# Optimization experiments

Measured on AMD Instinct MI355X. Metric: run time of the kernel, lower is better.

The kernel has to match this reference:

```python
import jax, jax.numpy as jnp
import numpy as np

NUM_HEADS = 4
HIDDEN = 384

def _l2norm(t, eps=1e-12):
    # torch.nn.functional.normalize(dim=-1): x / max(||x||_2, eps)
    n = jnp.sqrt(jnp.sum(t * t, axis=-1, keepdims=True))
    return t / jnp.maximum(n, eps)

def setup_inputs() -> dict:
    key = jax.random.key(0)
    k1, k2, k3, k4 = jax.random.split(key, 4)
    B, N, C = 4, 16384, HIDDEN
    x = jax.random.normal(k1, (B, N, C), dtype=jnp.float32)
    W_qkv = jax.random.normal(k2, (3 * C, C), dtype=jnp.float32) * 0.02  # torch Linear weight [out,in], no bias
    temperature_ch = jnp.ones((NUM_HEADS, 1, 1), dtype=jnp.float32)
    W_out = jax.random.normal(k3, (C, C), dtype=jnp.float32) * 0.02
    b_out = jax.random.normal(k4, (C,), dtype=jnp.float32) * 0.02
    return {"x": x, "W_qkv": W_qkv, "temperature_ch": temperature_ch,
            "W_out": W_out, "b_out": b_out,
            "B_in": 4, "C_in": C, "H": 32, "W": 32, "D": 16}

def reference(x, W_qkv, temperature_ch, W_out, b_out, B_in, C_in, H, W, D):
    B, N, C = x.shape
    h = NUM_HEADS
    d = C // h
    # qkv projection: (B,N,3C) -> (3,B,h,N,d)
    qkv = (x @ W_qkv.T).reshape(B, N, 3, h, d).transpose(2, 0, 3, 1, 4)
    q, k, v = qkv[0], qkv[1], qkv[2]
    # transpose token/channel axes: (B,h,d,N)
    q = jnp.swapaxes(q, -2, -1)
    k = jnp.swapaxes(k, -2, -1)
    v = jnp.swapaxes(v, -2, -1)
    # L2-normalize over tokens (last axis)
    q = _l2norm(q)
    k = _l2norm(k)
    # channel attention: (B,h,d,d)
    attn = jnp.einsum('bhcn,bhdn->bhcd', q, k)
    attn = attn * temperature_ch  # (h,1,1) broadcasts over (B,h,d,d)
    attn = jax.nn.softmax(attn, axis=-1)
    # (B,h,d,N) -> (B,N,h,d) -> (B,N,C)
    x_CA = jnp.einsum('bhcd,bhdn->bhcn', attn, v)
    x_CA = x_CA.transpose(0, 3, 1, 2).reshape(B, N, C)
    return x_CA @ W_out.T + b_out
```

## Files before the change

### kernel.cpp

```cpp
#include <hip/hip_runtime.h>
#include <math.h>


#define B_    4
#define NTOK  16384
#define C_    384
#define NH    4
#define DH    96

typedef __attribute__((ext_vector_type(8))) short short8;
typedef __attribute__((ext_vector_type(4))) float f32x4;
typedef __attribute__((ext_vector_type(4))) unsigned short ushort4v;
typedef __attribute__((ext_vector_type(8))) unsigned short ushort8v;
typedef __attribute__((ext_vector_type(4))) unsigned int uint4v;

#define XH_B   0ull
#define XHT_B  50331648ull
#define GP_B   100663296ull
#define G_B    138412032ull
#define P_B    140771328ull
#define SSQ_B  145489920ull
#define ATT_B  145502208ull
#define T_B    146092032ull
#define MPH_B  150810624ull

__device__ inline unsigned short f2bf(float f) {
    unsigned u = __float_as_uint(f);
    u += 0x7FFFu + ((u >> 16) & 1u);
    return (unsigned short)(u >> 16);
}

__device__ inline void load16(const void* g, void* l) {
    __builtin_amdgcn_global_load_lds(
        (const __attribute__((address_space(1))) unsigned int*)g,
        (__attribute__((address_space(3))) unsigned int*)l, 16, 0, 0);
}

__global__ __launch_bounds__(256) void k_conv(const float* __restrict__ X,
                                              unsigned short* __restrict__ Xh,
                                              unsigned short* __restrict__ XhT) {
    __shared__ __align__(16) unsigned int Tp[64 * 33];
    const int tid = threadIdx.x;
    const int t0 = blockIdx.x * 64, c0 = blockIdx.y * 64, b = blockIdx.z;
    const int tp = tid >> 4, cg = tid & 15;
#pragma unroll
    for (int i = 0; i < 2; ++i) {
        const int tpair = tp + 16 * i;
        const int t = t0 + tpair * 2;
        const float4 v0 = *(const float4*)(X + ((size_t)(b * NTOK + t))     * C_ + c0 + cg * 4);
        const float4 v1 = *(const float4*)(X + ((size_t)(b * NTOK + t + 1)) * C_ + c0 + cg * 4);
        const unsigned short h00 = f2bf(v0.x), h01 = f2bf(v0.y), h02 = f2bf(v0.z), h03 = f2bf(v0.w);
        const unsigned short h10 = f2bf(v1.x), h11 = f2bf(v1.y), h12 = f2bf(v1.z), h13 = f2bf(v1.w);
        ushort4v a; a.x = h00; a.y = h01; a.z = h02; a.w = h03;
        ushort4v c; c.x = h10; c.y = h11; c.z = h12; c.w = h13;
        *(ushort4v*)(Xh + ((size_t)(b * NTOK + t))     * C_ + c0 + cg * 4) = a;
        *(ushort4v*)(Xh + ((size_t)(b * NTOK + t + 1)) * C_ + c0 + cg * 4) = c;
        Tp[(cg * 4 + 0) * 33 + tpair] = (unsigned)h00 | ((unsigned)h10 << 16);
        Tp[(cg * 4 + 1) * 33 + tpair] = (unsigned)h01 | ((unsigned)h11 << 16);
        Tp[(cg * 4 + 2) * 33 + tpair] = (unsigned)h02 | ((unsigned)h12 << 16);
        Tp[(cg * 4 + 3) * 33 + tpair] = (unsigned)h03 | ((unsigned)h13 << 16);
    }
    __syncthreads();
    const int c = tid >> 2, seg = tid & 3;
    unsigned int w[8];
#pragma unroll
    for (int k = 0; k < 8; ++k) w[k] = Tp[c * 33 + seg * 8 + k];
    unsigned int* dst = (unsigned int*)(XhT + ((size_t)(b * C_ + c0 + c)) * NTOK + t0 + seg * 16);
    uint4v s0; s0.x = w[0]; s0.y = w[1]; s0.z = w[2]; s0.w = w[3];
    uint4v s1; s1.x = w[4]; s1.y = w[5]; s1.z = w[6]; s1.w = w[7];
    *(uint4v*)dst       = s0;
    *((uint4v*)dst + 1) = s1;
}

__global__ __launch_bounds__(256, 2) void k_gram_mfma(const unsigned short* __restrict__ XhT,
                                                      float* __restrict__ Gpart) {
    __shared__ __align__(16) unsigned char sm[32768];
    const int l = blockIdx.x;
    const int xcd = l & 7, slot = l >> 3;
    const int grp = xcd * 8 + slot / 6, tile = slot % 6;
    const int chunk = grp >> 2, b = grp & 3;
    const int ti = (tile == 0) ? 0 : (tile < 3 ? 1 : 2);
    const int tj = tile - (ti * (ti + 1)) / 2;
    const int tid = threadIdx.x;
    const int lane = tid & 63, wid = tid >> 6;
    const int wr = wid >> 1, wc = wid & 1;

    const int e = (lane & 7) ^ (lane >> 3);
    const int rsub = lane >> 3;

    const size_t rowb = (size_t)NTOK * 2;
    const unsigned char* Abase = (const unsigned char*)XhT + (size_t)(b * C_ + ti * 128) * rowb;
    const unsigned char* Bbase = (const unsigned char*)XhT + (size_t)(b * C_ + tj * 128) * rowb;

    f32x4 acc[4][4];
#pragma unroll
    for (int i = 0; i < 4; i++)
#pragma unroll
        for (int j = 0; j < 4; j++) acc[i][j] = (f32x4)(0.f);

    for (int ks = 0; ks < 16; ++ks) {
        const size_t colb = (size_t)(chunk * 1024 + ks * 64) * 2 + (size_t)e * 16;
        __syncthreads();
#pragma unroll
        for (int call = 0; call < 4; ++call) {
            const int row = wid * 32 + call * 8 + rsub;
            load16(Abase + (size_t)row * rowb + colb, sm + (wid * 32 + call * 8) * 128);
            load16(Bbase + (size_t)row * rowb + colb, sm + 16384 + (wid * 32 + call * 8) * 128);
        }
        __syncthreads();
#pragma unroll
        for (int p = 0; p < 2; ++p) {
            const int s = p * 4 + (lane >> 4);
            short8 av[4], bv[4];
#pragma unroll
            for (int fi = 0; fi < 4; ++fi) {
                const int c = wr * 64 + fi * 16 + (lane & 15);
                av[fi] = *(const short8*)(sm + c * 128 + ((s ^ (c & 7)) << 4));
            }
#pragma unroll
            for (int fj = 0; fj < 4; ++fj) {
                const int c = wc * 64 + fj * 16 + (lane & 15);
                bv[fj] = *(const short8*)(sm + 16384 + c * 128 + ((s ^ (c & 7)) << 4));
            }
#pragma unroll
            for (int fi = 0; fi < 4; ++fi)
#pragma unroll
                for (int fj = 0; fj < 4; ++fj)
                    acc[fi][fj] = __builtin_amdgcn_mfma_f32_16x16x32_bf16(av[fi], bv[fj], acc[fi][fj], 0, 0, 0);
        }
    }
    float* gp = Gpart + (size_t)grp * (C_ * C_);
    const int r0 = (lane >> 4) * 4, cc = lane & 15;
#pragma unroll
    for (int fi = 0; fi < 4; ++fi) {
        const int ci = ti * 128 + wr * 64 + fi * 16 + r0;
#pragma unroll
        for (int fj = 0; fj < 4; ++fj) {
            const int cj = tj * 128 + wc * 64 + fj * 16 + cc;
#pragma unroll
            for (int r = 0; r < 4; ++r)
                gp[(size_t)(ci + r) * C_ + cj] = acc[fi][fj][r];
        }
    }
    if (ti != tj) {
#pragma unroll
        for (int fi = 0; fi < 4; ++fi) {
            const int cib = ti * 128 + wr * 64 + fi * 16 + r0;
#pragma unroll
            for (int fj = 0; fj < 4; ++fj) {
                const int cjb = tj * 128 + wc * 64 + fj * 16 + cc;
                *(f32x4*)(gp + (size_t)cjb * C_ + cib) = acc[fi][fj];
            }
        }
    }
}

__global__ __launch_bounds__(256) void k_reduceG(const float* __restrict__ Gpart,
                                                 float* __restrict__ G) {
    const size_t eo = ((size_t)blockIdx.x * 256 + threadIdx.x) * 4;
    float4 s = *(const float4*)(Gpart + eo);
#pragma unroll
    for (int c = 1; c < 16; ++c) {
        const float4 v = *(const float4*)(Gpart + (size_t)c * (B_ * C_ * C_) + eo);
        s.x += v.x; s.y += v.y; s.z += v.z; s.w += v.w;
    }
    *(float4*)(G + eo) = s;
}

__global__ __launch_bounds__(256) void k_P64(const float* __restrict__ Wqkv,
                                             const float* __restrict__ G,
                                             float* __restrict__ P) {
    __shared__ float As[32][65];
    __shared__ float Bs[32][65];
    const int tid = threadIdx.x;
    const int sel = blockIdx.z & 1, b = blockIdx.z >> 1;
    const int m0 = blockIdx.x * 64, n0 = blockIdx.y * 64;
    const float* A  = Wqkv + (size_t)sel * C_ * C_;
    const float* Bm = G + (size_t)b * C_ * C_;
    const int lr = tid >> 2, lk = (tid & 3) * 8;
    const int tm = (tid & 15) * 4, tn = (tid >> 4) * 4;
    float acc[4][4];
#pragma unroll
    for (int i = 0; i < 4; i++)
#pragma unroll
        for (int j = 0; j < 4; j++) acc[i][j] = 0.f;

    for (int k0 = 0; k0 < C_; k0 += 32) {
        float4 a0 = *(const float4*)(A  + (size_t)(m0 + lr) * C_ + k0 + lk);
        float4 a1 = *(const float4*)(A  + (size_t)(m0 + lr) * C_ + k0 + lk + 4);
        float4 b0 = *(const float4*)(Bm + (size_t)(n0 + lr) * C_ + k0 + lk);
        float4 b1 = *(const float4*)(Bm + (size_t)(n0 + lr) * C_ + k0 + lk + 4);
        __syncthreads();
        As[lk + 0][lr] = a0.x; As[lk + 1][lr] = a0.y; As[lk + 2][lr] = a0.z; As[lk + 3][lr] = a0.w;
        As[lk + 4][lr] = a1.x; As[lk + 5][lr] = a1.y; As[lk + 6][lr] = a1.z; As[lk + 7][lr] = a1.w;
        Bs[lk + 0][lr] = b0.x; Bs[lk + 1][lr] = b0.y; Bs[lk + 2][lr] = b0.z; Bs[lk + 3][lr] = b0.w;
        Bs[lk + 4][lr] = b1.x; Bs[lk + 5][lr] = b1.y; Bs[lk + 6][lr] = b1.z; Bs[lk + 7][lr] = b1.w;
        __syncthreads();
#pragma unroll
        for (int k = 0; k < 32; k++) {
            float a[4], bb[4];
            *(float4*)&a[0]  = *(const float4*)&As[k][tm];
            *(float4*)&bb[0] = *(const float4*)&Bs[k][tn];
#pragma unroll
            for (int i = 0; i < 4; i++)
#pragma unroll
                for (int j = 0; j < 4; j++)
                    acc[i][j] = fmaf(a[i], bb[j], acc[i][j]);
        }
    }
    float* outp = P + ((size_t)(sel * B_ + b) * C_ + m0 + tm) * C_ + n0 + tn;
#pragma unroll
    for (int i = 0; i < 4; i++) {
        float4 c0 = make_float4(acc[i][0], acc[i][1], acc[i][2], acc[i][3]);
        *(float4*)(outp + (size_t)i * C_) = c0;
    }
}

__global__ __launch_bounds__(256) void k_diag(const float* __restrict__ P,
                                              const float* __restrict__ Wqkv,
                                              float* __restrict__ ssq) {
    int g = blockIdx.x * 256 + threadIdx.x;
    int sel = g / (B_ * C_), rem = g % (B_ * C_), b = rem / C_, c = rem % C_;
    const float* pr = P + ((size_t)(sel * B_ + b) * C_ + c) * C_;
    const float* wr = Wqkv + ((size_t)sel * C_ + c) * C_;
    float s = 0.f;
#pragma unroll 4
    for (int k = 0; k < C_; k += 4) {
        float4 pv = *(const float4*)(pr + k);
        float4 wv = *(const float4*)(wr + k);
        s += pv.x * wv.x + pv.y * wv.y + pv.z * wv.z + pv.w * wv.w;
    }
    ssq[g] = s;
}

__global__ __launch_bounds__(256) void k_S(const float* __restrict__ P,
                                           const float* __restrict__ Wqkv,
                                           float* __restrict__ S) {
    __shared__ float Ps[32 * 97];
    __shared__ float Ks[32 * 17];
    const int cs = blockIdx.x, bh = blockIdx.y;
    const int b = bh >> 2, h = bh & 3;
    const int tid = threadIdx.x;
    const int ti = tid & 15, tj = tid >> 4;
    const float* P1 = P + ((size_t)b * C_ + h * DH) * C_;
    const float* Wk = Wqkv + ((size_t)(C_ + h * DH + cs * 16)) * C_;
    float acc[6];
#pragma unroll
    for (int i = 0; i < 6; i++) acc[i] = 0.f;

    for (int k0 = 0; k0 < C_; k0 += 32) {
        __syncthreads();
#pragma unroll
        for (int j = 0; j < 3; j++) {
            int f = tid + 256 * j;
            int row = f >> 3, q = f & 7;
            float4 v = *(const float4*)(P1 + (size_t)row * C_ + k0 + q * 4);
            Ps[(q * 4 + 0) * 97 + row] = v.x;
            Ps[(q * 4 + 1) * 97 + row] = v.y;
            Ps[(q * 4 + 2) * 97 + row] = v.z;
            Ps[(q * 4 + 3) * 97 + row] = v.w;
        }
        {
            int row = tid >> 4, kk = (tid & 15) * 2;
            float2 w = *(const float2*)(Wk + (size_t)row * C_ + k0 + kk);
            Ks[(kk + 0) * 17 + row] = w.x;
            Ks[(kk + 1) * 17 + row] = w.y;
        }
        __syncthreads();
#pragma unroll
        for (int k = 0; k < 32; k++) {
            const float bb = Ks[k * 17 + tj];
#pragma unroll
            for (int i = 0; i < 6; i++)
                acc[i] = fmaf(Ps[k * 97 + ti * 6 + i], bb, acc[i]);
        }
    }
    float* Sb = S + (size_t)bh * DH * DH;
#pragma unroll
    for (int i = 0; i < 6; i++)
        Sb[(size_t)(ti * 6 + i) * DH + cs * 16 + tj] = acc[i];
}

__global__ __launch_bounds__(128) void k_soft(float* __restrict__ S,
                                              const float* __restrict__ ssq,
                                              const float* __restrict__ temp) {
    __shared__ float rnk[DH];
    const int bh = blockIdx.x;
    const int b = bh >> 2, h = bh & 3;
    const int r = threadIdx.x;
    if (r < DH)
        rnk[r] = 1.f / fmaxf(sqrtf(ssq[B_ * C_ + b * C_ + h * DH + r]), 1e-12f);
    __syncthreads();
    if (r >= DH) return;
    const float rnq = temp[h] / fmaxf(sqrtf(ssq[b * C_ + h * DH + r]), 1e-12f);
    float* row = S + (size_t)bh * DH * DH + (size_t)r * DH;
    float rv[DH];
    float m = -1e30f;
#pragma unroll
    for (int d = 0; d < DH; d++) {
        rv[d] = row[d] * rnq * rnk[d];
        m = fmaxf(m, rv[d]);
    }
    float s = 0.f;
#pragma unroll
    for (int d = 0; d < DH; d++) { rv[d] = __expf(rv[d] - m); s += rv[d]; }
    const float inv = 1.f / s;
#pragma unroll
    for (int d = 0; d < DH; d++) row[d] = rv[d] * inv;
}

__global__ __launch_bounds__(128) void k_T(const float* __restrict__ attn,
                                           const float* __restrict__ Wqkv,
                                           float* __restrict__ T) {
    const int ck = blockIdx.x * 128 + threadIdx.x;
    const int y = blockIdx.y;
    const int b = y / C_, hc = y % C_, h = hc / DH, c = hc % DH;
    const float* ar = attn + ((size_t)(b * NH + h) * DH + c) * DH;
    const float* wv = Wqkv + ((size_t)(2 * C_ + h * DH)) * C_ + ck;
    float s = 0.f;
#pragma unroll 8
    for (int d = 0; d < DH; d++) s = fmaf(ar[d], wv[(size_t)d * C_], s);
    T[((size_t)b * C_ + hc) * C_ + ck] = s;
}

__global__ __launch_bounds__(256) void k_Mp64(const float* __restrict__ Wout,
                                              const float* __restrict__ T,
                                              unsigned short* __restrict__ Mph) {
    __shared__ float As[32][65];
    __shared__ float Bs[32][65];
    const int tid = threadIdx.x;
    const int b = blockIdx.z;
    const int m0 = blockIdx.x * 64, n0 = blockIdx.y * 64;
    const float* Tb = T + (size_t)b * C_ * C_;
    const int la_r = tid >> 2, la_k = (tid & 3) * 8;
    const int lb_k = tid >> 3, lb_c = (tid & 7) * 8;
    const int tm = (tid & 15) * 4, tn = (tid >> 4) * 4;
    float acc[4][4];
#pragma unroll
    for (int i = 0; i < 4; i++)
#pragma unroll
        for (int j = 0; j < 4; j++) acc[i][j] = 0.f;

    for (int k0 = 0; k0 < C_; k0 += 32) {
        float4 a0 = *(const float4*)(Wout + (size_t)(m0 + la_r) * C_ + k0 + la_k);
        float4 a1 = *(const float4*)(Wout + (size_t)(m0 + la_r) * C_ + k0 + la_k + 4);
        float4 b0 = *(const float4*)(Tb + (size_t)(k0 + lb_k) * C_ + n0 + lb_c);
        float4 b1 = *(const float4*)(Tb + (size_t)(k0 + lb_k) * C_ + n0 + lb_c + 4);
        __syncthreads();
        As[la_k + 0][la_r] = a0.x; As[la_k + 1][la_r] = a0.y; As[la_k + 2][la_r] = a0.z; As[la_k + 3][la_r] = a0.w;
        As[la_k + 4][la_r] = a1.x; As[la_k + 5][la_r] = a1.y; As[la_k + 6][la_r] = a1.z; As[la_k + 7][la_r] = a1.w;
        *(float4*)&Bs[lb_k][lb_c]     = b0;
        *(float4*)&Bs[lb_k][lb_c + 4] = b1;
        __syncthreads();
#pragma unroll
        for (int k = 0; k < 32; k++) {
            float a[4], bb[4];
            *(float4*)&a[0]  = *(const float4*)&As[k][tm];
            *(float4*)&bb[0] = *(const float4*)&Bs[k][tn];
#pragma unroll
            for (int i = 0; i < 4; i++)
#pragma unroll
                for (int j = 0; j < 4; j++)
                    acc[i][j] = fmaf(a[i], bb[j], acc[i][j]);
        }
    }
    unsigned short* outp = Mph + ((size_t)b * C_ + m0 + tm) * C_ + n0 + tn;
#pragma unroll
    for (int i = 0; i < 4; i++) {
        ushort4v h4;
        h4.x = f2bf(acc[i][0]); h4.y = f2bf(acc[i][1]);
        h4.z = f2bf(acc[i][2]); h4.w = f2bf(acc[i][3]);
        *(ushort4v*)(outp + (size_t)i * C_) = h4;
    }
}

__global__ __launch_bounds__(256, 2) void k_out_mfma(const unsigned short* __restrict__ Xh,
                                                     const unsigned short* __restrict__ Mph,
                                                     const float* __restrict__ bias,
                                                     float* __restrict__ out) {
    __shared__ __align__(16) unsigned char sm[32768];
    const int l = blockIdx.x;
    const int xcd = l & 7, k = l >> 3;
    const int mblk = xcd * 64 + k / 3, nblk = k % 3;
    const int m0 = mblk * 128, i0 = nblk * 128;
    const int b = mblk >> 7;
    const int tid = threadIdx.x;
    const int lane = tid & 63, wid = tid >> 6;
    const int wr = wid >> 1, wc = wid & 1;

    const int e = (lane & 7) ^ (lane >> 3);
    const int rsub = lane >> 3;

    const unsigned char* Abase = (const unsigned char*)Xh + (size_t)m0 * (C_ * 2);
    const unsigned char* Bbase = (const unsigned char*)Mph + (size_t)b * (C_ * C_ * 2) + (size_t)i0 * (C_ * 2);

    f32x4 acc[4][4];
#pragma unroll
    for (int i = 0; i < 4; i++)
#pragma unroll
        for (int j = 0; j < 4; j++) acc[i][j] = (f32x4)(0.f);

    for (int ks = 0; ks < 6; ++ks) {
        const size_t colb = (size_t)ks * 128 + (size_t)e * 16;
        __syncthreads();
#pragma unroll
        for (int call = 0; call < 4; ++call) {
            const int row = wid * 32 + call * 8 + rsub;
            load16(Abase + (size_t)row * (C_ * 2) + colb, sm + (wid * 32 + call * 8) * 128);
            load16(Bbase + (size_t)row * (C_ * 2) + colb, sm + 16384 + (wid * 32 + call * 8) * 128);
        }
        __syncthreads();
#pragma unroll
        for (int p = 0; p < 2; ++p) {
            const int s = p * 4 + (lane >> 4);
            short8 av[4], bv[4];
#pragma unroll
            for (int fi = 0; fi < 4; ++fi) {
                const int c = wr * 64 + fi * 16 + (lane & 15);
                av[fi] = *(const short8*)(sm + c * 128 + ((s ^ (c & 7)) << 4));
            }
#pragma unroll
            for (int fj = 0; fj < 4; ++fj) {
                const int c = wc * 64 + fj * 16 + (lane & 15);
                bv[fj] = *(const short8*)(sm + 16384 + c * 128 + ((s ^ (c & 7)) << 4));
            }
#pragma unroll
            for (int fi = 0; fi < 4; ++fi)
#pragma unroll
                for (int fj = 0; fj < 4; ++fj)
                    acc[fi][fj] = __builtin_amdgcn_mfma_f32_16x16x32_bf16(av[fi], bv[fj], acc[fi][fj], 0, 0, 0);
        }
    }
    const int r0 = (lane >> 4) * 4, cc = lane & 15;
#pragma unroll
    for (int fi = 0; fi < 4; ++fi) {
        const int m = m0 + wr * 64 + fi * 16 + r0;
#pragma unroll
        for (int fj = 0; fj < 4; ++fj) {
            const int ii = i0 + wc * 64 + fj * 16 + cc;
            const float bi = bias[ii];
#pragma unroll
            for (int r = 0; r < 4; ++r)
                out[(size_t)(m + r) * C_ + ii] = acc[fi][fj][r] + bi;
        }
    }
}

extern "C" void kernel_launch(void* const* d_in, const int* in_sizes, int n_in,
                              void* d_out, int out_size, void* d_ws, size_t ws_size,
                              hipStream_t stream) {
    const float* x    = (const float*)d_in[0];
    const float* Wqkv = (const float*)d_in[1];
    const float* temp = (const float*)d_in[2];
    const float* Wout = (const float*)d_in[3];
    const float* bout = (const float*)d_in[4];
    float* out = (float*)d_out;

    unsigned char* w8 = (unsigned char*)d_ws;
    unsigned short* Xh  = (unsigned short*)(w8 + XH_B);
    unsigned short* XhT = (unsigned short*)(w8 + XHT_B);
    float* Gpart = (float*)(w8 + GP_B);
    float* G     = (float*)(w8 + G_B);
    float* P     = (float*)(w8 + P_B);
    float* ssq   = (float*)(w8 + SSQ_B);
    float* Satt  = (float*)(w8 + ATT_B);
    float* T     = (float*)(w8 + T_B);
    unsigned short* Mph = (unsigned short*)(w8 + MPH_B);

    k_conv     <<<dim3(256, 6, B_), 256, 0, stream>>>(x, Xh, XhT);
    k_gram_mfma<<<dim3(384), 256, 0, stream>>>(XhT, Gpart);
    k_reduceG  <<<dim3(576), 256, 0, stream>>>(Gpart, G);
    k_P64      <<<dim3(6, 6, 2 * B_), 256, 0, stream>>>(Wqkv, G, P);
    k_diag     <<<dim3(12), 256, 0, stream>>>(P, Wqkv, ssq);
    k_S        <<<dim3(6, B_ * NH), 256, 0, stream>>>(P, Wqkv, Satt);
    k_soft     <<<dim3(B_ * NH), 128, 0, stream>>>(Satt, ssq, temp);
    k_T        <<<dim3(3, B_ * C_), 128, 0, stream>>>(Satt, Wqkv, T);
    k_Mp64     <<<dim3(6, 6, B_), 256, 0, stream>>>(Wout, T, Mph);
    k_out_mfma <<<dim3(1536), 256, 0, stream>>>(Xh, Mph, bout, out);
}
```

Measured before the change: 411.6 us.

## Split fp32-to-bf16 conversion from transpose and fold row-norm diag into softmax

Replaces the combined convert+transpose kernel with a flat grid-stride fp32-to-bf16 conversion kernel and a separate transpose kernel that reads the bf16 copy in 128x128 tiles. The aim is fully coalesced streaming of the fp32 input and wider transpose stores. It also removes the k_diag launch by computing the q/k squared norms inside k_soft, saving a launch but making 16 small blocks do the dot products serially. The extra pass re-reads the bf16 copy, which adds memory traffic.

```diff
diff --git a/kernel.cpp b/kernel.cpp
--- a/kernel.cpp
+++ b/kernel.cpp
@@ -19,7 +19,6 @@
 #define GP_B   100663296ull
 #define G_B    138412032ull
 #define P_B    140771328ull
-#define SSQ_B  145489920ull
 #define ATT_B  145502208ull
 #define T_B    146092032ull
 #define MPH_B  150810624ull
@@ -36,40 +35,50 @@
         (__attribute__((address_space(3))) unsigned int*)l, 16, 0, 0);
 }
 
-__global__ __launch_bounds__(256) void k_conv(const float* __restrict__ X,
-                                              unsigned short* __restrict__ Xh,
-                                              unsigned short* __restrict__ XhT) {
-    __shared__ __align__(16) unsigned int Tp[64 * 33];
-    const int tid = threadIdx.x;
-    const int t0 = blockIdx.x * 64, c0 = blockIdx.y * 64, b = blockIdx.z;
-    const int tp = tid >> 4, cg = tid & 15;
-#pragma unroll
-    for (int i = 0; i < 2; ++i) {
-        const int tpair = tp + 16 * i;
-        const int t = t0 + tpair * 2;
-        const float4 v0 = *(const float4*)(X + ((size_t)(b * NTOK + t))     * C_ + c0 + cg * 4);
-        const float4 v1 = *(const float4*)(X + ((size_t)(b * NTOK + t + 1)) * C_ + c0 + cg * 4);
-        const unsigned short h00 = f2bf(v0.x), h01 = f2bf(v0.y), h02 = f2bf(v0.z), h03 = f2bf(v0.w);
-        const unsigned short h10 = f2bf(v1.x), h11 = f2bf(v1.y), h12 = f2bf(v1.z), h13 = f2bf(v1.w);
-        ushort4v a; a.x = h00; a.y = h01; a.z = h02; a.w = h03;
-        ushort4v c; c.x = h10; c.y = h11; c.z = h12; c.w = h13;
-        *(ushort4v*)(Xh + ((size_t)(b * NTOK + t))     * C_ + c0 + cg * 4) = a;
-        *(ushort4v*)(Xh + ((size_t)(b * NTOK + t + 1)) * C_ + c0 + cg * 4) = c;
-        Tp[(cg * 4 + 0) * 33 + tpair] = (unsigned)h00 | ((unsigned)h10 << 16);
-        Tp[(cg * 4 + 1) * 33 + tpair] = (unsigned)h01 | ((unsigned)h11 << 16);
-        Tp[(cg * 4 + 2) * 33 + tpair] = (unsigned)h02 | ((unsigned)h12 << 16);
-        Tp[(cg * 4 + 3) * 33 + tpair] = (unsigned)h03 | ((unsigned)h13 << 16);
+__global__ __launch_bounds__(256) void k_convS(const float* __restrict__ X,
+                                               unsigned short* __restrict__ Xh) {
+    const size_t n4 = (size_t)B_ * NTOK * C_ / 4;
+    const size_t stride = (size_t)gridDim.x * 256;
+    for (size_t i = (size_t)blockIdx.x * 256 + threadIdx.x; i < n4; i += stride) {
+        const float4 v = *(const float4*)(X + i * 4);
+        ushort4v h;
+        h.x = f2bf(v.x); h.y = f2bf(v.y); h.z = f2bf(v.z); h.w = f2bf(v.w);
+        *(ushort4v*)(Xh + i * 4) = h;
+    }
+}
+
+__global__ __launch_bounds__(256) void k_trans(const unsigned short* __restrict__ Xh,
+                                               unsigned short* __restrict__ XhT) {
+    __shared__ unsigned int Tp[64 * 129];
+    const int tid = threadIdx.x;
+    const int t0 = blockIdx.x * 128, c0 = blockIdx.y * 128, b = blockIdx.z;
+    const int cg = tid & 15;
+#pragma unroll
+    for (int p = 0; p < 4; ++p) {
+        const int tp = (tid >> 4) + 16 * p;
+        const int t = t0 + tp * 2;
+        const ushort8v r0 = *(const ushort8v*)(Xh + ((size_t)(b * NTOK + t))     * C_ + c0 + cg * 8);
+        const ushort8v r1 = *(const ushort8v*)(Xh + ((size_t)(b * NTOK + t + 1)) * C_ + c0 + cg * 8);
+#pragma unroll
+        for (int j = 0; j < 8; ++j)
+            Tp[tp * 129 + cg * 8 + j] = (unsigned)r0[j] | ((unsigned)r1[j] << 16);
     }
     __syncthreads();
-    const int c = tid >> 2, seg = tid & 3;
-    unsigned int w[8];
-#pragma unroll
-    for (int k = 0; k < 8; ++k) w[k] = Tp[c * 33 + seg * 8 + k];
-    unsigned int* dst = (unsigned int*)(XhT + ((size_t)(b * C_ + c0 + c)) * NTOK + t0 + seg * 16);
-    uint4v s0; s0.x = w[0]; s0.y = w[1]; s0.z = w[2]; s0.w = w[3];
-    uint4v s1; s1.x = w[4]; s1.y = w[5]; s1.z = w[6]; s1.w = w[7];
-    *(uint4v*)dst       = s0;
-    *((uint4v*)dst + 1) = s1;
+    const int qtr = tid & 3;
+#pragma unroll
+    for (int p = 0; p < 2; ++p) {
+        const int c = (tid >> 2) + 64 * p;
+        unsigned int w[16];
+#pragma unroll
+        for (int m = 0; m < 16; ++m)
+            w[m] = Tp[(qtr * 16 + m) * 129 + c];
+        unsigned int* dst = (unsigned int*)(XhT + ((size_t)(b * C_ + c0 + c)) * NTOK + t0 + qtr * 32);
+#pragma unroll
+        for (int i = 0; i < 4; ++i) {
+            uint4v s4; s4.x = w[i*4+0]; s4.y = w[i*4+1]; s4.z = w[i*4+2]; s4.w = w[i*4+3];
+            *((uint4v*)dst + i) = s4;
+        }
+    }
 }
 
 __global__ __launch_bounds__(256, 2) void k_gram_mfma(const unsigned short* __restrict__ XhT,
@@ -216,23 +225,6 @@
     }
 }
 
-__global__ __launch_bounds__(256) void k_diag(const float* __restrict__ P,
-                                              const float* __restrict__ Wqkv,
-                                              float* __restrict__ ssq) {
-    int g = blockIdx.x * 256 + threadIdx.x;
-    int sel = g / (B_ * C_), rem = g % (B_ * C_), b = rem / C_, c = rem % C_;
-    const float* pr = P + ((size_t)(sel * B_ + b) * C_ + c) * C_;
-    const float* wr = Wqkv + ((size_t)sel * C_ + c) * C_;
-    float s = 0.f;
-#pragma unroll 4
-    for (int k = 0; k < C_; k += 4) {
-        float4 pv = *(const float4*)(pr + k);
-        float4 wv = *(const float4*)(wr + k);
-        s += pv.x * wv.x + pv.y * wv.y + pv.z * wv.z + pv.w * wv.w;
-    }
-    ssq[g] = s;
-}
-
 __global__ __launch_bounds__(256) void k_S(const float* __restrict__ P,
                                            const float* __restrict__ Wqkv,
                                            float* __restrict__ S) {
@@ -282,17 +274,39 @@
 }
 
 __global__ __launch_bounds__(128) void k_soft(float* __restrict__ S,
-                                              const float* __restrict__ ssq,
+                                              const float* __restrict__ P,
+                                              const float* __restrict__ Wqkv,
                                               const float* __restrict__ temp) {
     __shared__ float rnk[DH];
     const int bh = blockIdx.x;
     const int b = bh >> 2, h = bh & 3;
     const int r = threadIdx.x;
-    if (r < DH)
-        rnk[r] = 1.f / fmaxf(sqrtf(ssq[B_ * C_ + b * C_ + h * DH + r]), 1e-12f);
+    if (r < DH) {
+        const float* p2 = P + ((size_t)(B_ + b) * C_ + h * DH + r) * C_;
+        const float* wk = Wqkv + ((size_t)(C_ + h * DH + r)) * C_;
+        float s = 0.f;
+#pragma unroll 4
+        for (int k = 0; k < C_; k += 4) {
+            const float4 pv = *(const float4*)(p2 + k);
+            const float4 wv = *(const float4*)(wk + k);
+            s += pv.x * wv.x + pv.y * wv.y + pv.z * wv.z + pv.w * wv.w;
+        }
+        rnk[r] = 1.f / fmaxf(sqrtf(s), 1e-12f);
+    }
     __syncthreads();
     if (r >= DH) return;
-    const float rnq = temp[h] / fmaxf(sqrtf(ssq[b * C_ + h * DH + r]), 1e-12f);
+    float sq = 0.f;
+    {
+        const float* p1 = P + ((size_t)b * C_ + h * DH + r) * C_;
+        const float* wq = Wqkv + ((size_t)(h * DH + r)) * C_;
+#pragma unroll 4
+        for (int k = 0; k < C_; k += 4) {
+            const float4 pv = *(const float4*)(p1 + k);
+            const float4 wv = *(const float4*)(wq + k);
+            sq += pv.x * wv.x + pv.y * wv.y + pv.z * wv.z + pv.w * wv.w;
+        }
+    }
+    const float rnq = temp[h] / fmaxf(sqrtf(sq), 1e-12f);
     float* row = S + (size_t)bh * DH * DH + (size_t)r * DH;
     float rv[DH];
     float m = -1e30f;
@@ -462,18 +476,17 @@
     float* Gpart = (float*)(w8 + GP_B);
     float* G     = (float*)(w8 + G_B);
     float* P     = (float*)(w8 + P_B);
-    float* ssq   = (float*)(w8 + SSQ_B);
     float* Satt  = (float*)(w8 + ATT_B);
     float* T     = (float*)(w8 + T_B);
     unsigned short* Mph = (unsigned short*)(w8 + MPH_B);
 
-    k_conv     <<<dim3(256, 6, B_), 256, 0, stream>>>(x, Xh, XhT);
+    k_convS    <<<dim3(2048), 256, 0, stream>>>(x, Xh);
+    k_trans    <<<dim3(128, 3, B_), 256, 0, stream>>>(Xh, XhT);
     k_gram_mfma<<<dim3(384), 256, 0, stream>>>(XhT, Gpart);
     k_reduceG  <<<dim3(576), 256, 0, stream>>>(Gpart, G);
     k_P64      <<<dim3(6, 6, 2 * B_), 256, 0, stream>>>(Wqkv, G, P);
-    k_diag     <<<dim3(12), 256, 0, stream>>>(P, Wqkv, ssq);
     k_S        <<<dim3(6, B_ * NH), 256, 0, stream>>>(P, Wqkv, Satt);
-    k_soft     <<<dim3(B_ * NH), 128, 0, stream>>>(Satt, ssq, temp);
+    k_soft     <<<dim3(B_ * NH), 128, 0, stream>>>(Satt, P, Wqkv, temp);
     k_T        <<<dim3(3, B_ * C_), 128, 0, stream>>>(Satt, Wqkv, T);
     k_Mp64     <<<dim3(6, 6, B_), 256, 0, stream>>>(Wout, T, Mph);
     k_out_mfma <<<dim3(1536), 256, 0, stream>>>(Xh, Mph, bout, out);
```

After: 390.1 us. 5.2% less time.
